# Optimization experiments

Measured on AMD Instinct MI355X. Metric: run time of the kernel, lower is better.

## Reference

```python
import jax, jax.numpy as jnp
import numpy as np

GRID_NUM = 3  # pykan 'grid' (number of intervals)
K = 3         # spline order

def bspline_basis(x, grid, k):
    # Cox-de Boor recursion, matching pykan B_batch with a shared extended grid.
    # x: (N, Din); grid: (G,) extended grid with G = GRID_NUM + 2*k + 1
    x = x[..., None]  # (N, Din, 1)
    B = ((x >= grid[:-1]) & (x < grid[1:])).astype(x.dtype)  # (N, Din, G-1)
    for p in range(1, k + 1):
        left = (x - grid[:-(p + 1)]) / (grid[p:-1] - grid[:-(p + 1)])
        right = (grid[p + 1:] - x) / (grid[p + 1:] - grid[1:-p])
        B = left * B[..., :-1] + right * B[..., 1:]
    return B  # (N, Din, GRID_NUM + k)

def setup_inputs() -> dict:
    key = jax.random.key(0)
    k1, k2, k3 = jax.random.split(key, 3)
    Bsz, S, Din, Dout = 4, 2048, 768, 768
    x = jax.random.normal(k1, (Bsz, S, Din), dtype=jnp.float32)
    # noise-scale-like init for spline coefficients (noise_scale=0.1)
    coef = (0.1 / GRID_NUM) * jax.random.normal(k2, (Dout, Din, GRID_NUM + K), dtype=jnp.float32)
    inv_sqrt_in = np.float32(1.0 / np.sqrt(Din))
    scale_base = inv_sqrt_in + 0.1 * inv_sqrt_in * jax.random.normal(k3, (Dout, Din), dtype=jnp.float32)
    scale_sp = jnp.ones((Dout, Din), dtype=jnp.float32)
    bias = jnp.zeros((Dout,), dtype=jnp.float32)
    return {"x": x, "coef": coef, "scale_base": scale_base, "scale_sp": scale_sp, "bias": bias}

def reference(x, coef, scale_base, scale_sp, bias):
    # x: (B, S, Din) -> flatten tokens as the original module does
    Bsz, S, Din = x.shape
    xf = x.reshape(-1, Din)  # (N, Din)
    # extended grid: linspace(-1,1,GRID_NUM+1) extended by K points each side (h = 2/GRID_NUM)
    h = 2.0 / GRID_NUM
    grid = jnp.arange(-K, GRID_NUM + K + 1, dtype=x.dtype) * h - 1.0  # (GRID_NUM + 2K + 1,)
    basis = bspline_basis(xf, grid, K)  # (N, Din, GRID_NUM+K)
    # per-edge activation: scale_base*silu(x) + scale_sp*spline(x); mask==1; symbolic branch==0
    base = jax.nn.silu(xf) @ scale_base.T  # (N, Dout)
    spline = jnp.einsum('nim,oim->no', basis, scale_sp[:, :, None] * coef)  # (N, Dout)
    out = base + spline + bias  # bias from pykan biases[l].weight
    return out.reshape(Bsz, S, -1)
```

## Files before the change

kernel.cpp:

```cpp
#include <hip/hip_runtime.h>
#include <hip/hip_bf16.h>


typedef _Float16 f16;
typedef __attribute__((ext_vector_type(8))) _Float16 f16x8;
typedef __attribute__((ext_vector_type(4))) float f32x4;

#define NTOK 8192
#define DIN 768
#define DOUT 768
#define KAUG 5376
#define BM 128
#define BN 128
#define BK 32
#define KT (KAUG / BK)

typedef __attribute__((address_space(1))) void gvoid;
typedef __attribute__((address_space(3))) void lvoid;

__global__ __launch_bounds__(256) void build_A(const float* __restrict__ x,
                                               f16* __restrict__ Aa) {
  int idx = blockIdx.x * 256 + threadIdx.x;
  float xv = x[idx];
  int n = idx / DIN;
  int i = idx - n * DIN;

  float s = xv / (1.0f + __expf(-xv));

  const float h = 2.0f / 3.0f;
  float B[9];
#pragma unroll
  for (int g = 0; g < 9; ++g) {
    float t0 = (float)(g - 3) * h - 1.0f;
    float t1 = (float)(g - 2) * h - 1.0f;
    B[g] = (xv >= t0 && xv < t1) ? 1.0f : 0.0f;
  }
#pragma unroll
  for (int p = 1; p <= 3; ++p) {
    float inv = 1.0f / ((float)p * h);
#pragma unroll
    for (int j = 0; j < 9 - 3; ++j) {
      if (j < 9 - p) {
        float tj = (float)(j - 3) * h - 1.0f;
        float tjp1 = (float)(j + p + 1 - 3) * h - 1.0f;
        B[j] = (xv - tj) * inv * B[j] + (tjp1 - xv) * inv * B[j + 1];
      }
    }
#pragma unroll
    for (int j = 6; j < 9; ++j) {
      if (j < 9 - p) {
        float tj = (float)(j - 3) * h - 1.0f;
        float tjp1 = (float)(j + p + 1 - 3) * h - 1.0f;
        B[j] = (xv - tj) * inv * B[j] + (tjp1 - xv) * inv * B[j + 1];
      }
    }
  }

  size_t base = (size_t)n * KAUG + i;
  Aa[base] = (f16)s;
#pragma unroll
  for (int m = 0; m < 6; ++m) Aa[base + (size_t)(m + 1) * DIN] = (f16)B[m];
}

__global__ __launch_bounds__(256) void build_W(const float* __restrict__ sb,
                                               const float* __restrict__ ssp,
                                               const float* __restrict__ coef,
                                               f16* __restrict__ Wa) {
  int idx = blockIdx.x * 256 + threadIdx.x;
  float b = sb[idx];
  float sp = ssp[idx];
  int o = idx / DIN;
  int i = idx - o * DIN;
  size_t base = (size_t)o * KAUG + i;
  Wa[base] = (f16)b;
#pragma unroll
  for (int m = 0; m < 6; ++m)
    Wa[base + (size_t)(m + 1) * DIN] = (f16)(sp * coef[(size_t)idx * 6 + m]);
}

__global__ __launch_bounds__(256) void kan_gemm(const f16* __restrict__ A,
                                                const f16* __restrict__ W,
                                                const float* __restrict__ bias,
                                                float* __restrict__ out) {
  __shared__ alignas(16) f16 As[BM * BK];
  __shared__ alignas(16) f16 Bs[BN * BK];

  const int tid = threadIdx.x;
  const int wave = tid >> 6;
  const int lane = tid & 63;
  const int m0 = blockIdx.y * BM;
  const int n0 = blockIdx.x * BN;
  const int wm = (wave >> 1) * 64;
  const int wn = (wave & 1) * 64;
  const int r = lane & 15;
  const int q = lane >> 4;

  f32x4 acc[4][4] = {};

  const int c0 = wave * 64 + lane;
  const int rowA0 = c0 >> 2, kb0 = c0 & 3;
  const int c1 = c0 + 256;
  const int rowA1 = c1 >> 2, kb1 = c1 & 3;

  const f16* gA0 = A + (size_t)(m0 + rowA0) * KAUG + kb0 * 8;
  const f16* gA1 = A + (size_t)(m0 + rowA1) * KAUG + kb1 * 8;
  const f16* gB0 = W + (size_t)(n0 + rowA0) * KAUG + kb0 * 8;
  const f16* gB1 = W + (size_t)(n0 + rowA1) * KAUG + kb1 * 8;

  f16* ldsA = As + wave * 512;
  f16* ldsB = Bs + wave * 512;

  for (int kt = 0; kt < KT; ++kt) {
    const int koff = kt * BK;
    __builtin_amdgcn_global_load_lds((gvoid*)(gA0 + koff), (lvoid*)(ldsA), 16, 0, 0);
    __builtin_amdgcn_global_load_lds((gvoid*)(gA1 + koff), (lvoid*)(ldsA + 2048), 16, 0, 0);
    __builtin_amdgcn_global_load_lds((gvoid*)(gB0 + koff), (lvoid*)(ldsB), 16, 0, 0);
    __builtin_amdgcn_global_load_lds((gvoid*)(gB1 + koff), (lvoid*)(ldsB + 2048), 16, 0, 0);
    __syncthreads();

    f16x8 af[4], bf[4];
#pragma unroll
    for (int mi = 0; mi < 4; ++mi)
      af[mi] = *(const f16x8*)&As[(wm + mi * 16 + r) * BK + q * 8];
#pragma unroll
    for (int ni = 0; ni < 4; ++ni)
      bf[ni] = *(const f16x8*)&Bs[(wn + ni * 16 + r) * BK + q * 8];
#pragma unroll
    for (int mi = 0; mi < 4; ++mi)
#pragma unroll
      for (int ni = 0; ni < 4; ++ni)
        acc[mi][ni] =
            __builtin_amdgcn_mfma_f32_16x16x32_f16(af[mi], bf[ni], acc[mi][ni], 0, 0, 0);
    __syncthreads();
  }

#pragma unroll
  for (int mi = 0; mi < 4; ++mi) {
#pragma unroll
    for (int ni = 0; ni < 4; ++ni) {
      const int gcol = n0 + wn + ni * 16 + r;
      const float bv = bias[gcol];
#pragma unroll
      for (int rg = 0; rg < 4; ++rg) {
        const int grow = m0 + wm + mi * 16 + q * 4 + rg;
        out[(size_t)grow * DOUT + gcol] = acc[mi][ni][rg] + bv;
      }
    }
  }
}

extern "C" void kernel_launch(void* const* d_in, const int* in_sizes, int n_in,
                              void* d_out, int out_size, void* d_ws, size_t ws_size,
                              hipStream_t stream) {
  const float* x = (const float*)d_in[0];
  const float* coef = (const float*)d_in[1];
  const float* scale_base = (const float*)d_in[2];
  const float* scale_sp = (const float*)d_in[3];
  const float* bias = (const float*)d_in[4];
  float* out = (float*)d_out;

  f16* Aa = (f16*)d_ws;
  f16* Wa = (f16*)((char*)d_ws + (size_t)NTOK * KAUG * 2);

  build_A<<<(NTOK * DIN) / 256, 256, 0, stream>>>(x, Aa);
  build_W<<<(DOUT * DIN) / 256, 256, 0, stream>>>(scale_base, scale_sp, coef, Wa);
  kan_gemm<<<dim3(DOUT / BN, NTOK / BM), 256, 0, stream>>>(Aa, Wa, bias, out);
}
```

Baseline: 222.4 us.

## Double-buffer LDS tiles in GEMM and vectorize spline basis construction

New measurement: 221.9 us. No clear change (-0.2%).

```diff
diff --git a/kernel.cpp b/kernel.cpp
--- a/kernel.cpp
+++ b/kernel.cpp
@@ -1,8 +1,8 @@
 #include <hip/hip_runtime.h>
-#include <hip/hip_bf16.h>
 
 
 typedef _Float16 f16;
+typedef __attribute__((ext_vector_type(4))) _Float16 f16x4;
 typedef __attribute__((ext_vector_type(8))) _Float16 f16x8;
 typedef __attribute__((ext_vector_type(4))) float f32x4;
 
@@ -18,48 +18,54 @@
 typedef __attribute__((address_space(1))) void gvoid;
 typedef __attribute__((address_space(3))) void lvoid;
 
-__global__ __launch_bounds__(256) void build_A(const float* __restrict__ x,
-                                               f16* __restrict__ Aa) {
-  int idx = blockIdx.x * 256 + threadIdx.x;
-  float xv = x[idx];
-  int n = idx / DIN;
-  int i = idx - n * DIN;
-
-  float s = xv / (1.0f + __expf(-xv));
-
+__device__ __forceinline__ void spline6(float xv, float* __restrict__ B, float& s) {
+  s = xv / (1.0f + __expf(-xv));
   const float h = 2.0f / 3.0f;
-  float B[9];
+  float Bb[9];
 #pragma unroll
   for (int g = 0; g < 9; ++g) {
     float t0 = (float)(g - 3) * h - 1.0f;
     float t1 = (float)(g - 2) * h - 1.0f;
-    B[g] = (xv >= t0 && xv < t1) ? 1.0f : 0.0f;
+    Bb[g] = (xv >= t0 && xv < t1) ? 1.0f : 0.0f;
   }
 #pragma unroll
   for (int p = 1; p <= 3; ++p) {
     float inv = 1.0f / ((float)p * h);
 #pragma unroll
-    for (int j = 0; j < 9 - 3; ++j) {
+    for (int j = 0; j < 8; ++j) {
       if (j < 9 - p) {
         float tj = (float)(j - 3) * h - 1.0f;
         float tjp1 = (float)(j + p + 1 - 3) * h - 1.0f;
-        B[j] = (xv - tj) * inv * B[j] + (tjp1 - xv) * inv * B[j + 1];
-      }
-    }
-#pragma unroll
-    for (int j = 6; j < 9; ++j) {
-      if (j < 9 - p) {
-        float tj = (float)(j - 3) * h - 1.0f;
-        float tjp1 = (float)(j + p + 1 - 3) * h - 1.0f;
-        B[j] = (xv - tj) * inv * B[j] + (tjp1 - xv) * inv * B[j + 1];
+        Bb[j] = (xv - tj) * inv * Bb[j] + (tjp1 - xv) * inv * Bb[j + 1];
       }
     }
   }
+#pragma unroll
+  for (int m = 0; m < 6; ++m) B[m] = Bb[m];
+}
+
+__global__ __launch_bounds__(256) void build_A(const float* __restrict__ x,
+                                               f16* __restrict__ Aa) {
+  int idx = (blockIdx.x * 256 + threadIdx.x) * 4;
+  float4 xv = *(const float4*)(x + idx);
+  int n = idx / DIN;
+  int i = idx - n * DIN;
+
+  float B0[6], B1[6], B2[6], B3[6];
+  float s0, s1, s2, s3;
+  spline6(xv.x, B0, s0);
+  spline6(xv.y, B1, s1);
+  spline6(xv.z, B2, s2);
+  spline6(xv.w, B3, s3);
 
   size_t base = (size_t)n * KAUG + i;
-  Aa[base] = (f16)s;
+  f16x4 sv = {(f16)s0, (f16)s1, (f16)s2, (f16)s3};
+  *(f16x4*)(Aa + base) = sv;
 #pragma unroll
-  for (int m = 0; m < 6; ++m) Aa[base + (size_t)(m + 1) * DIN] = (f16)B[m];
+  for (int m = 0; m < 6; ++m) {
+    f16x4 bv = {(f16)B0[m], (f16)B1[m], (f16)B2[m], (f16)B3[m]};
+    *(f16x4*)(Aa + base + (size_t)(m + 1) * DIN) = bv;
+  }
 }
 
 __global__ __launch_bounds__(256) void build_W(const float* __restrict__ sb,
@@ -82,8 +88,10 @@
                                                 const f16* __restrict__ W,
                                                 const float* __restrict__ bias,
                                                 float* __restrict__ out) {
-  __shared__ alignas(16) f16 As[BM * BK];
-  __shared__ alignas(16) f16 Bs[BN * BK];
+  __shared__ alignas(16) f16 As0[BM * BK];
+  __shared__ alignas(16) f16 As1[BM * BK];
+  __shared__ alignas(16) f16 Bs0[BN * BK];
+  __shared__ alignas(16) f16 Bs1[BN * BK];
 
   const int tid = threadIdx.x;
   const int wave = tid >> 6;
@@ -107,32 +115,47 @@
   const f16* gB0 = W + (size_t)(n0 + rowA0) * KAUG + kb0 * 8;
   const f16* gB1 = W + (size_t)(n0 + rowA1) * KAUG + kb1 * 8;
 
-  f16* ldsA = As + wave * 512;
-  f16* ldsB = Bs + wave * 512;
+  const int wo = wave * 512;
 
-  for (int kt = 0; kt < KT; ++kt) {
-    const int koff = kt * BK;
-    __builtin_amdgcn_global_load_lds((gvoid*)(gA0 + koff), (lvoid*)(ldsA), 16, 0, 0);
-    __builtin_amdgcn_global_load_lds((gvoid*)(gA1 + koff), (lvoid*)(ldsA + 2048), 16, 0, 0);
-    __builtin_amdgcn_global_load_lds((gvoid*)(gB0 + koff), (lvoid*)(ldsB), 16, 0, 0);
-    __builtin_amdgcn_global_load_lds((gvoid*)(gB1 + koff), (lvoid*)(ldsB + 2048), 16, 0, 0);
+#define STAGE(AS, BS, ktile)                                                             \
+  do {                                                                                   \
+    const int koff = (ktile)*BK;                                                         \
+    __builtin_amdgcn_global_load_lds((gvoid*)(gA0 + koff), (lvoid*)(AS + wo), 16, 0, 0); \
+    __builtin_amdgcn_global_load_lds((gvoid*)(gA1 + koff), (lvoid*)(AS + wo + 2048), 16, \
+                                     0, 0);                                              \
+    __builtin_amdgcn_global_load_lds((gvoid*)(gB0 + koff), (lvoid*)(BS + wo), 16, 0, 0); \
+    __builtin_amdgcn_global_load_lds((gvoid*)(gB1 + koff), (lvoid*)(BS + wo + 2048), 16, \
+                                     0, 0);                                              \
+  } while (0)
+
+#define COMPUTE(AS, BS)                                                                  \
+  do {                                                                                   \
+    f16x8 af[4], bf[4];                                                                  \
+    _Pragma("unroll") for (int mi = 0; mi < 4; ++mi) af[mi] =                            \
+        *(const f16x8*)&AS[(wm + mi * 16 + r) * BK + q * 8];                             \
+    _Pragma("unroll") for (int ni = 0; ni < 4; ++ni) bf[ni] =                            \
+        *(const f16x8*)&BS[(wn + ni * 16 + r) * BK + q * 8];                             \
+    _Pragma("unroll") for (int mi = 0; mi < 4; ++mi) _Pragma("unroll") for (int ni = 0;  \
+                                                                            ni < 4;     \
+                                                                            ++ni)       \
+        acc[mi][ni] =                                                                    \
+        __builtin_amdgcn_mfma_f32_16x16x32_f16(af[mi], bf[ni], acc[mi][ni], 0, 0, 0);    \
+  } while (0)
+
+  STAGE(As0, Bs0, 0);
+  __syncthreads();
+
+  for (int kt = 0; kt < KT; kt += 2) {
+    STAGE(As1, Bs1, kt + 1);
+    COMPUTE(As0, Bs0);
     __syncthreads();
-
-    f16x8 af[4], bf[4];
-#pragma unroll
-    for (int mi = 0; mi < 4; ++mi)
-      af[mi] = *(const f16x8*)&As[(wm + mi * 16 + r) * BK + q * 8];
-#pragma unroll
-    for (int ni = 0; ni < 4; ++ni)
-      bf[ni] = *(const f16x8*)&Bs[(wn + ni * 16 + r) * BK + q * 8];
-#pragma unroll
-    for (int mi = 0; mi < 4; ++mi)
-#pragma unroll
-      for (int ni = 0; ni < 4; ++ni)
-        acc[mi][ni] =
-            __builtin_amdgcn_mfma_f32_16x16x32_f16(af[mi], bf[ni], acc[mi][ni], 0, 0, 0);
+    if (kt + 2 < KT) STAGE(As0, Bs0, kt + 2);
+    COMPUTE(As1, Bs1);
     __syncthreads();
   }
+
+#undef STAGE
+#undef COMPUTE
 
 #pragma unroll
   for (int mi = 0; mi < 4; ++mi) {
@@ -162,7 +185,7 @@
   f16* Aa = (f16*)d_ws;
   f16* Wa = (f16*)((char*)d_ws + (size_t)NTOK * KAUG * 2);
 
-  build_A<<<(NTOK * DIN) / 256, 256, 0, stream>>>(x, Aa);
+  build_A<<<(NTOK * DIN) / (256 * 4), 256, 0, stream>>>(x, Aa);
   build_W<<<(DOUT * DIN) / 256, 256, 0, stream>>>(scale_base, scale_sp, coef, Wa);
   kan_gemm<<<dim3(DOUT / BN, NTOK / BM), 256, 0, stream>>>(Aa, Wa, bias, out);
 }
```
